# Performance work log

Measured on AMD Instinct MI355X. Metric: run time of the kernel, lower is better.

The kernel has to match this reference:

```python
import jax, jax.numpy as jnp
import numpy as np

D = 1024
H = 16
HD = D // H
FF = 4096
EPS = 1e-5
B, L = 8, 1024

def setup_inputs() -> dict:
    key = jax.random.key(0)
    ks = jax.random.split(key, 12)
    s = lambda k, shape: jax.random.normal(k, shape, dtype=jnp.float32) * (shape[0] ** -0.5)
    return {
        "x": jax.random.normal(ks[0], (B, L, D), dtype=jnp.float32),
        "attention_mask": jnp.ones((B, L), dtype=jnp.int32),
        "wq": s(ks[1], (D, D)), "bq": jnp.zeros((D,), jnp.float32),
        "wk": s(ks[2], (D, D)), "bk": jnp.zeros((D,), jnp.float32),
        "wv": s(ks[3], (D, D)), "bv": jnp.zeros((D,), jnp.float32),
        "wo": s(ks[4], (D, D)), "bo": jnp.zeros((D,), jnp.float32),
        "ln1_s": jnp.ones((D,), jnp.float32), "ln1_b": jnp.zeros((D,), jnp.float32),
        "ln2_s": jnp.ones((D,), jnp.float32), "ln2_b": jnp.zeros((D,), jnp.float32),
        "w1": s(ks[5], (D, FF)), "b1": jnp.zeros((FF,), jnp.float32),
        "w2": s(ks[6], (FF, D)), "b2": jnp.zeros((D,), jnp.float32),
    }

def _layer_norm(x, scale, bias):
    mu = jnp.mean(x, axis=-1, keepdims=True)
    var = jnp.mean(jnp.square(x - mu), axis=-1, keepdims=True)
    return (x - mu) * jax.lax.rsqrt(var + EPS) * scale + bias

def _quick_gelu(x):
    return x * jax.nn.sigmoid(1.702 * x)

def reference(x, attention_mask, wq, bq, wk, bk, wv, bv, wo, bo,
              ln1_s, ln1_b, ln2_s, ln2_b, w1, b1, w2, b2):
    Bc, Lc, Dc = x.shape
    scale = HD ** -0.5
    # --- attention block (pre-LN) ---
    h = _layer_norm(x, ln1_s, ln1_b)
    to_heads = lambda t: t.reshape(Bc, Lc, H, HD).transpose(0, 2, 1, 3)
    q = to_heads(h @ wq + bq)
    k = to_heads(h @ wk + bk)
    v = to_heads(h @ wv + bv)
    scores = jnp.einsum('bhqd,bhkd->bhqk', q.astype(jnp.float32), k.astype(jnp.float32)) * scale
    fmask = jnp.where(attention_mask[:, None, None, :] > 0, 0.0,
                      jnp.finfo(scores.dtype).min)
    weights = jax.nn.softmax(scores + fmask, axis=-1)
    attn = jnp.einsum('bhqk,bhkd->bhqd', weights, v.astype(jnp.float32))
    attn = attn.transpose(0, 2, 1, 3).reshape(Bc, Lc, Dc).astype(x.dtype)
    x = x + (attn @ wo + bo)
    # --- MLP block (pre-LN) ---
    h = _layer_norm(x, ln2_s, ln2_b)
    h = _quick_gelu(h @ w1 + b1) @ w2 + b2
    return x + h
```

## Files before the change

### kernel.cpp

```cpp
#include <hip/hip_runtime.h>
#include <math.h>

#define D_MODEL 1024
#define N_TOK   8192
#define SEQ_L   1024
#define N_HEAD  16
#define HEAD_D  64
#define FF_DIM  4096

typedef __attribute__((ext_vector_type(8))) short bf16x8;
typedef __attribute__((ext_vector_type(4))) short short4v;
typedef __attribute__((ext_vector_type(2))) int  int2v;
typedef __attribute__((ext_vector_type(4))) float f32x4;

#define MFMA16(a, b, c) __builtin_amdgcn_mfma_f32_16x16x32_bf16((a), (b), (c), 0, 0, 0)

#define GLD16(gp, lp) __builtin_amdgcn_global_load_lds(                      \
    (const __attribute__((address_space(1))) void*)(gp),                     \
    (__attribute__((address_space(3))) void*)(lp), 16, 0, 0)

#if defined(__has_builtin)
#if __has_builtin(__builtin_amdgcn_exp2f)
#define EXP2F(x) __builtin_amdgcn_exp2f(x)
#else
#define EXP2F(x) exp2f(x)
#endif
#else
#define EXP2F(x) exp2f(x)
#endif

__device__ __forceinline__ short f2bf(float f) {
    unsigned u = __float_as_uint(f);
    u += 0x7fffu + ((u >> 16) & 1u);
    return (short)(u >> 16);
}

__device__ __forceinline__ int pack2bf(float a, float b) {
    unsigned ua = __float_as_uint(a) + 0x8000u;
    unsigned ub = __float_as_uint(b) + 0x8000u;
    return __builtin_amdgcn_perm(ub, ua, 0x07060302u);
}

__global__ __launch_bounds__(256) void ln_kernel(const float* __restrict__ x,
                                                 const float* __restrict__ g,
                                                 const float* __restrict__ b,
                                                 short* __restrict__ o)
{
    int t = blockIdx.x;
    const float* xr = x + (size_t)t * D_MODEL;
    short* orow = o + (size_t)t * D_MODEL;
    float vals[4];
    float lsum = 0.f, lsq = 0.f;
#pragma unroll
    for (int i = 0; i < 4; i++) {
        float v = xr[threadIdx.x + i * 256];
        vals[i] = v; lsum += v; lsq += v * v;
    }
#pragma unroll
    for (int off = 32; off > 0; off >>= 1) {
        lsum += __shfl_down(lsum, off);
        lsq  += __shfl_down(lsq,  off);
    }
    __shared__ float red[8];
    int wid = threadIdx.x >> 6, lane = threadIdx.x & 63;
    if (lane == 0) { red[wid] = lsum; red[4 + wid] = lsq; }
    __syncthreads();
    if (threadIdx.x == 0) {
        red[0] = red[0] + red[1] + red[2] + red[3];
        red[4] = red[4] + red[5] + red[6] + red[7];
    }
    __syncthreads();
    float mean = red[0] * (1.f / D_MODEL);
    float var  = red[4] * (1.f / D_MODEL) - mean * mean;
    float inv  = rsqrtf(var + 1e-5f);
#pragma unroll
    for (int i = 0; i < 4; i++) {
        int c = threadIdx.x + i * 256;
        orow[c] = f2bf((vals[i] - mean) * inv * g[c] + b[c]);
    }
}

__global__ __launch_bounds__(256) void prep_kernel(
    const float* __restrict__ wq, const float* __restrict__ wk,
    const float* __restrict__ wv, const float* __restrict__ wo,
    const float* __restrict__ w1, const float* __restrict__ w2,
    const int*   __restrict__ amask,
    short* __restrict__ wqkvt, short* __restrict__ wot,
    short* __restrict__ w1t,  short* __restrict__ w2t,
    float* __restrict__ fmask)
{
    int id = blockIdx.x;
    if (id >= 12288) {
        int i = (id - 12288) * 256 + threadIdx.x;
        fmask[i] = (amask[i] > 0) ? 0.f : -1e30f;
        return;
    }
    const float* src; short* dst; int R, C, tloc, csh;
    if (id < 4096) {
        int wsel = id >> 10; tloc = id & 1023; R = 1024; C = 1024; csh = 5;
        src = (wsel == 0) ? wq : (wsel == 1) ? wk : (wsel == 2) ? wv : wo;
        dst = (wsel == 3) ? wot : (wqkvt + (size_t)wsel * 1024 * 1024);
    } else if (id < 8192) {
        tloc = id - 4096; R = 1024; C = 4096; csh = 7; src = w1; dst = w1t;
    } else {
        tloc = id - 8192; R = 4096; C = 1024; csh = 5; src = w2; dst = w2t;
    }
    int ty = tloc >> csh, tx = tloc & ((1 << csh) - 1);
    int r0 = ty * 32, c0 = tx * 32;
    __shared__ float t[32][33];
    int tid = threadIdx.x;
#pragma unroll
    for (int i = 0; i < 4; i++) {
        int idx = i * 256 + tid;
        int r = idx >> 5, c = idx & 31;
        t[r][c] = src[(size_t)(r0 + r) * C + c0 + c];
    }
    __syncthreads();
#pragma unroll
    for (int i = 0; i < 4; i++) {
        int idx = i * 256 + tid;
        int rr = idx >> 5, cc = idx & 31;
        dst[(size_t)(c0 + rr) * R + r0 + cc] = f2bf(t[cc][rr]);
    }
}

template<int DBUF>
__global__ __launch_bounds__(256) void gemm_bf16(
    const short* __restrict__ A, int lda,
    const short* __restrict__ Bt, int ldb,
    const float* __restrict__ bias,
    const float* __restrict__ bias2,
    const float* __restrict__ bias3,
    const float* __restrict__ resid,
    float* __restrict__ Cf, short* __restrict__ Cb, short* __restrict__ Cvt,
    int ldc, int K, int act, int qkv, int gx)
{
    __shared__ __align__(16) short sA[(1 + DBUF) * 8192];
    __shared__ __align__(16) short sB[(1 + DBUF) * 8192];
    const int tid = threadIdx.x;
    const int lane = tid & 63, wave = tid >> 6;
    const int quad = lane >> 4, l15 = lane & 15;

    const int id = blockIdx.x;
    const int xcd = id & 7, j = id >> 3;
    const int bx = j % gx, by = xcd + 8 * (j / gx);
    const int bm = by * 128, bn = bx * 128;
    const int wm = (wave >> 1) * 64, wn = (wave & 1) * 64;

    const int lr = lane >> 3;
    const int lc = (lane & 7) ^ lr;
    const int sw = l15 & 7;

    const short* Ab = A  + (size_t)(bm + wave * 32 + lr) * lda + lc * 8;
    const short* Bb = Bt + (size_t)(bn + wave * 32 + lr) * ldb + lc * 8;

    f32x4 acc[4][4];
#pragma unroll
    for (int i = 0; i < 4; i++)
#pragma unroll
        for (int jj = 0; jj < 4; jj++) acc[i][jj] = (f32x4){0.f, 0.f, 0.f, 0.f};

    const int nk = K >> 6;

    if (DBUF) {
#pragma unroll
        for (int c = 0; c < 4; c++) {
            int cid = wave * 4 + c;
            GLD16(Ab + (size_t)(c * 8) * lda, &sA[cid * 512]);
            GLD16(Bb + (size_t)(c * 8) * ldb, &sB[cid * 512]);
        }
    }

    for (int ki = 0; ki < nk; ki++) {
        __syncthreads();
        if (DBUF) {
            if (ki + 1 < nk) {
                int k0 = (ki + 1) << 6, nb = (ki + 1) & 1;
#pragma unroll
                for (int c = 0; c < 4; c++) {
                    int cid = wave * 4 + c;
                    GLD16(Ab + (size_t)(c * 8) * lda + k0, &sA[nb * 8192 + cid * 512]);
                    GLD16(Bb + (size_t)(c * 8) * ldb + k0, &sB[nb * 8192 + cid * 512]);
                }
            }
        } else {
            int k0 = ki << 6;
#pragma unroll
            for (int c = 0; c < 4; c++) {
                int cid = wave * 4 + c;
                GLD16(Ab + (size_t)(c * 8) * lda + k0, &sA[cid * 512]);
                GLD16(Bb + (size_t)(c * 8) * ldb + k0, &sB[cid * 512]);
            }
            __syncthreads();
        }
        const short* cA = &sA[DBUF ? (ki & 1) * 8192 : 0];
        const short* cB = &sB[DBUF ? (ki & 1) * 8192 : 0];
#pragma unroll
        for (int ko = 0; ko < 2; ko++) {
            bf16x8 af[4], bfr[4];
#pragma unroll
            for (int mt = 0; mt < 4; mt++) {
                int row = wm + mt * 16 + l15;
                af[mt] = *(const bf16x8*)&cA[(row * 8 + ((ko * 4 + quad) ^ sw)) * 8];
            }
#pragma unroll
            for (int nt = 0; nt < 4; nt++) {
                int row = wn + nt * 16 + l15;
                bfr[nt] = *(const bf16x8*)&cB[(row * 8 + ((ko * 4 + quad) ^ sw)) * 8];
            }
#pragma unroll
            for (int mt = 0; mt < 4; mt++)
#pragma unroll
                for (int nt = 0; nt < 4; nt++)
                    acc[mt][nt] = MFMA16(af[mt], bfr[nt], acc[mt][nt]);
        }
    }

#pragma unroll
    for (int mt = 0; mt < 4; mt++)
#pragma unroll
        for (int nt = 0; nt < 4; nt++) {
            int row0 = bm + wm + mt * 16 + quad * 4;
            int col  = bn + wn + nt * 16 + l15;
            if (qkv) {
                int seg = col >> 10, cloc = col & 1023;
                const float* bp = (seg == 0) ? bias : (seg == 1) ? bias2 : bias3;
                float bval = bp[cloc];
                if (seg == 2) {
                    int bb = row0 >> 10, l0 = row0 & 1023;
                    size_t page = (size_t)(bb * N_HEAD + (cloc >> 6)) * HEAD_D + (cloc & 63);
                    short4v pk = { f2bf(acc[mt][nt][0] + bval), f2bf(acc[mt][nt][1] + bval),
                                   f2bf(acc[mt][nt][2] + bval), f2bf(acc[mt][nt][3] + bval) };
                    *(short4v*)&Cvt[page * SEQ_L + l0] = pk;
                } else {
                    short* dst = Cb + (size_t)seg * ((size_t)N_TOK * D_MODEL);
#pragma unroll
                    for (int r = 0; r < 4; r++)
                        dst[(size_t)(row0 + r) * D_MODEL + cloc] = f2bf(acc[mt][nt][r] + bval);
                }
            } else {
#pragma unroll
                for (int r = 0; r < 4; r++) {
                    int row = row0 + r;
                    float v = acc[mt][nt][r] + bias[col];
                    if (act) v = v / (1.f + __expf(-1.702f * v));
                    if (resid) v += resid[(size_t)row * ldc + col];
                    if (Cb) Cb[(size_t)row * ldc + col] = f2bf(v);
                    else    Cf[(size_t)row * ldc + col] = v;
                }
            }
        }
}

__global__ __launch_bounds__(256) void attn_kernel(
    const short* __restrict__ Q, const short* __restrict__ Kb,
    const short* __restrict__ Vt, const float* __restrict__ fmask,
    short* __restrict__ O)
{
    __shared__ __align__(16) short sK[8192];
    __shared__ __align__(16) short sV[8192];
    __shared__ __align__(16) short sP[4][16 * 136];
    __shared__ __align__(16) float sAl[4][20];

    const int g = blockIdx.x;
    const int xcd = g & 7, slot = g >> 3;
    const int qt = slot & 15, bhl = slot >> 4;
    const int bh = xcd * 16 + bhl;
    const int b = bh >> 4, h = bh & 15;

    const int tid = threadIdx.x;
    const int wave = tid >> 6, lane = tid & 63;
    const int quad = lane >> 4, l15 = lane & 15;

    const int qbase = b * SEQ_L + qt * 64;
    const short* qp = Q + (size_t)(qbase + wave * 16 + l15) * D_MODEL + h * HEAD_D + quad * 8;
    bf16x8 qf0 = *(const bf16x8*)qp;
    bf16x8 qf1 = *(const bf16x8*)(qp + 32);

    const short* Kbh = Kb + (size_t)b * SEQ_L * D_MODEL + h * HEAD_D;
    const short* Vbh = Vt + (size_t)(b * N_HEAD + h) * HEAD_D * SEQ_L;
    const float* mk  = fmask + b * SEQ_L;

    f32x4 o4[4];
#pragma unroll
    for (int nt = 0; nt < 4; nt++) o4[nt] = (f32x4){0.f, 0.f, 0.f, 0.f};
    float mrow = -1e30f, lrow = 0.f;
    short* pslab = &sP[wave][0];
    const float CSC = 0.125f * 1.4426950408889634f;

    for (int kt = 0; kt < SEQ_L / 128; kt++) {
        __syncthreads();
#pragma unroll
        for (int j = 0; j < 4; j++) {
            int cid = wave * 4 + j;
            int kc = cid >> 1, key0 = (cid & 1) << 6;
            GLD16(Kbh + (size_t)(kt * 128 + key0 + lane) * D_MODEL + kc * 8,
                  &sK[cid * 512]);
            GLD16(Vbh + (size_t)lane * SEQ_L + kt * 128 + cid * 8,
                  &sV[cid * 512]);
        }
        __syncthreads();

        f32x4 mkv[8];
#pragma unroll
        for (int sub = 0; sub < 8; sub++)
            mkv[sub] = *(const f32x4*)&mk[kt * 128 + sub * 16 + quad * 4];

        f32x4 s[8];
#pragma unroll
        for (int sub = 0; sub < 8; sub++) {
            bf16x8 kf0 = *(const bf16x8*)&sK[(quad * 128 + sub * 16 + l15) * 8];
            bf16x8 kf1 = *(const bf16x8*)&sK[((quad + 4) * 128 + sub * 16 + l15) * 8];
            s[sub] = (f32x4){0.f, 0.f, 0.f, 0.f};
            s[sub] = MFMA16(kf0, qf0, s[sub]);
            s[sub] = MFMA16(kf1, qf1, s[sub]);
        }
#pragma unroll
        for (int sub = 0; sub < 8; sub++)
#pragma unroll
            for (int r = 0; r < 4; r++) s[sub][r] = s[sub][r] * CSC + mkv[sub][r];

        f32x4 mx4 = s[0];
#pragma unroll
        for (int sub = 1; sub < 8; sub++)
#pragma unroll
            for (int r = 0; r < 4; r++) mx4[r] = fmaxf(mx4[r], s[sub][r]);
        float pmax = fmaxf(fmaxf(mx4[0], mx4[1]), fmaxf(mx4[2], mx4[3]));
        pmax = fmaxf(pmax, __shfl_xor(pmax, 16));
        pmax = fmaxf(pmax, __shfl_xor(pmax, 32));
        float mnew = fmaxf(mrow, pmax);
        float alpha = EXP2F(mrow - mnew);
        mrow = mnew;
        if (quad == 0) sAl[wave][l15] = alpha;

        float ls = 0.f;
#pragma unroll
        for (int sub = 0; sub < 8; sub++) {
            float p0 = EXP2F(s[sub][0] - mnew);
            float p1 = EXP2F(s[sub][1] - mnew);
            float p2 = EXP2F(s[sub][2] - mnew);
            float p3 = EXP2F(s[sub][3] - mnew);
            ls += (p0 + p1) + (p2 + p3);
            int2v pk = { pack2bf(p0, p1), pack2bf(p2, p3) };
            *(int2v*)&pslab[l15 * 136 + sub * 16 + quad * 4] = pk;
        }
        ls += __shfl_xor(ls, 16);
        ls += __shfl_xor(ls, 32);
        lrow = lrow * alpha + ls;

        f32x4 av = *(const f32x4*)&sAl[wave][quad * 4];
#pragma unroll
        for (int nt = 0; nt < 4; nt++)
#pragma unroll
            for (int r = 0; r < 4; r++) o4[nt][r] *= av[r];

        bf16x8 pf[4];
#pragma unroll
        for (int c = 0; c < 4; c++)
            pf[c] = *(const bf16x8*)&pslab[l15 * 136 + c * 32 + quad * 8];
#pragma unroll
        for (int nt = 0; nt < 4; nt++)
#pragma unroll
            for (int c = 0; c < 4; c++) {
                bf16x8 vfr = *(const bf16x8*)&sV[((c * 4 + quad) * 64 + nt * 16 + l15) * 8];
                o4[nt] = MFMA16(pf[c], vfr, o4[nt]);
            }
    }
    if (quad == 0) sAl[wave][l15] = 1.f / lrow;
    __syncthreads();
    f32x4 iv = *(const f32x4*)&sAl[wave][quad * 4];
#pragma unroll
    for (int nt = 0; nt < 4; nt++)
#pragma unroll
        for (int r = 0; r < 4; r++)
            O[(size_t)(qbase + wave * 16 + quad * 4 + r) * D_MODEL
              + h * HEAD_D + nt * 16 + l15] = f2bf(o4[nt][r] * iv[r]);
}

extern "C" void kernel_launch(void* const* d_in, const int* in_sizes, int n_in,
                              void* d_out, int out_size, void* d_ws, size_t ws_size,
                              hipStream_t stream)
{
    const float* x     = (const float*)d_in[0];
    const int*   amask = (const int*)  d_in[1];
    const float* wq    = (const float*)d_in[2];
    const float* bq    = (const float*)d_in[3];
    const float* wk    = (const float*)d_in[4];
    const float* bk    = (const float*)d_in[5];
    const float* wv    = (const float*)d_in[6];
    const float* bv    = (const float*)d_in[7];
    const float* wo    = (const float*)d_in[8];
    const float* bo    = (const float*)d_in[9];
    const float* ln1s  = (const float*)d_in[10];
    const float* ln1b  = (const float*)d_in[11];
    const float* ln2s  = (const float*)d_in[12];
    const float* ln2b  = (const float*)d_in[13];
    const float* w1    = (const float*)d_in[14];
    const float* b1    = (const float*)d_in[15];
    const float* w2    = (const float*)d_in[16];
    const float* b2    = (const float*)d_in[17];
    float* out = (float*)d_out;

    char* w = (char*)d_ws;
    short* wqkvt = (short*)(w + (size_t)0);
    short* wot   = (short*)(w + ((size_t)6  << 20));
    short* w1t   = (short*)(w + ((size_t)8  << 20));
    short* w2t   = (short*)(w + ((size_t)16 << 20));
    short* hb    = (short*)(w + ((size_t)24 << 20));
    short* qb    = (short*)(w + ((size_t)40 << 20));
    short* kbf   = (short*)(w + ((size_t)56 << 20));
    short* attnb = (short*)(w + ((size_t)72 << 20));
    short* vtb   = (short*)(w + ((size_t)88 << 20));
    short* ffb   = qb;
    float* fmaskb = (float*)d_out;

    dim3 blk(256);

    prep_kernel<<<dim3(12320), blk, 0, stream>>>(wq, wk, wv, wo, w1, w2, amask,
                                                 wqkvt, wot, w1t, w2t, fmaskb);

    ln_kernel<<<N_TOK, blk, 0, stream>>>(x, ln1s, ln1b, hb);

    gemm_bf16<0><<<dim3(24 * 64), blk, 0, stream>>>(
        hb, 1024, wqkvt, 1024, bq, bk, bv, nullptr,
        nullptr, qb, vtb, 1024, 1024, 0, 1, 24);

    attn_kernel<<<dim3(2048), blk, 0, stream>>>(qb, kbf, vtb, fmaskb, attnb);

    gemm_bf16<1><<<dim3(8 * 64), blk, 0, stream>>>(
        attnb, 1024, wot, 1024, bo, nullptr, nullptr, x,
        out, nullptr, nullptr, 1024, 1024, 0, 0, 8);

    ln_kernel<<<N_TOK, blk, 0, stream>>>(out, ln2s, ln2b, hb);

    gemm_bf16<0><<<dim3(32 * 64), blk, 0, stream>>>(
        hb, 1024, w1t, 1024, b1, nullptr, nullptr, nullptr,
        nullptr, ffb, nullptr, 4096, 1024, 1, 0, 32);
    gemm_bf16<1><<<dim3(8 * 64), blk, 0, stream>>>(
        ffb, 4096, w2t, 4096, b2, nullptr, nullptr, out,
        out, nullptr, nullptr, 1024, 4096, 0, 0, 8);
}
```

Measured before the change: 554.8 us.

## Process two 16-row query tiles per wave in attention kernel

Each wave now handles 32 query rows instead of 16, so the block covers 128 queries and the grid halves to 1024 blocks. Every K/V tile loaded into shared memory and every K/V fragment read from LDS is reused for two query tiles, which halves the global K/V traffic and LDS fragment reads per query. The cost is more accumulator and score registers per thread (possibly lower occupancy), a larger P slab in shared memory, and fewer blocks to fill the GPU.

```diff
diff --git a/kernel.cpp b/kernel.cpp
--- a/kernel.cpp
+++ b/kernel.cpp
@@ -259,12 +259,12 @@
 {
     __shared__ __align__(16) short sK[8192];
     __shared__ __align__(16) short sV[8192];
-    __shared__ __align__(16) short sP[4][16 * 136];
-    __shared__ __align__(16) float sAl[4][20];
+    __shared__ __align__(16) short sP[4][32 * 136];
+    __shared__ __align__(16) float sAl[4][2][20];
 
     const int g = blockIdx.x;
     const int xcd = g & 7, slot = g >> 3;
-    const int qt = slot & 15, bhl = slot >> 4;
+    const int qt = slot & 7, bhl = slot >> 3;
     const int bh = xcd * 16 + bhl;
     const int b = bh >> 4, h = bh & 15;
 
@@ -272,19 +272,26 @@
     const int wave = tid >> 6, lane = tid & 63;
     const int quad = lane >> 4, l15 = lane & 15;
 
-    const int qbase = b * SEQ_L + qt * 64;
-    const short* qp = Q + (size_t)(qbase + wave * 16 + l15) * D_MODEL + h * HEAD_D + quad * 8;
-    bf16x8 qf0 = *(const bf16x8*)qp;
-    bf16x8 qf1 = *(const bf16x8*)(qp + 32);
+    const int qbase = b * SEQ_L + qt * 128;
+    bf16x8 qf[2][2];
+#pragma unroll
+    for (int qh = 0; qh < 2; qh++) {
+        const short* qp = Q + (size_t)(qbase + wave * 32 + qh * 16 + l15) * D_MODEL
+                        + h * HEAD_D + quad * 8;
+        qf[qh][0] = *(const bf16x8*)qp;
+        qf[qh][1] = *(const bf16x8*)(qp + 32);
+    }
 
     const short* Kbh = Kb + (size_t)b * SEQ_L * D_MODEL + h * HEAD_D;
     const short* Vbh = Vt + (size_t)(b * N_HEAD + h) * HEAD_D * SEQ_L;
     const float* mk  = fmask + b * SEQ_L;
 
-    f32x4 o4[4];
-#pragma unroll
-    for (int nt = 0; nt < 4; nt++) o4[nt] = (f32x4){0.f, 0.f, 0.f, 0.f};
-    float mrow = -1e30f, lrow = 0.f;
+    f32x4 o4[2][4];
+#pragma unroll
+    for (int qh = 0; qh < 2; qh++)
+#pragma unroll
+        for (int nt = 0; nt < 4; nt++) o4[qh][nt] = (f32x4){0.f, 0.f, 0.f, 0.f};
+    float mrow[2] = {-1e30f, -1e30f}, lrow[2] = {0.f, 0.f};
     short* pslab = &sP[wave][0];
     const float CSC = 0.125f * 1.4426950408889634f;
 
@@ -306,75 +313,94 @@
         for (int sub = 0; sub < 8; sub++)
             mkv[sub] = *(const f32x4*)&mk[kt * 128 + sub * 16 + quad * 4];
 
-        f32x4 s[8];
+        f32x4 s[8][2];
 #pragma unroll
         for (int sub = 0; sub < 8; sub++) {
             bf16x8 kf0 = *(const bf16x8*)&sK[(quad * 128 + sub * 16 + l15) * 8];
             bf16x8 kf1 = *(const bf16x8*)&sK[((quad + 4) * 128 + sub * 16 + l15) * 8];
-            s[sub] = (f32x4){0.f, 0.f, 0.f, 0.f};
-            s[sub] = MFMA16(kf0, qf0, s[sub]);
-            s[sub] = MFMA16(kf1, qf1, s[sub]);
-        }
-#pragma unroll
-        for (int sub = 0; sub < 8; sub++)
-#pragma unroll
-            for (int r = 0; r < 4; r++) s[sub][r] = s[sub][r] * CSC + mkv[sub][r];
-
-        f32x4 mx4 = s[0];
-#pragma unroll
-        for (int sub = 1; sub < 8; sub++)
-#pragma unroll
-            for (int r = 0; r < 4; r++) mx4[r] = fmaxf(mx4[r], s[sub][r]);
-        float pmax = fmaxf(fmaxf(mx4[0], mx4[1]), fmaxf(mx4[2], mx4[3]));
-        pmax = fmaxf(pmax, __shfl_xor(pmax, 16));
-        pmax = fmaxf(pmax, __shfl_xor(pmax, 32));
-        float mnew = fmaxf(mrow, pmax);
-        float alpha = EXP2F(mrow - mnew);
-        mrow = mnew;
-        if (quad == 0) sAl[wave][l15] = alpha;
-
-        float ls = 0.f;
-#pragma unroll
-        for (int sub = 0; sub < 8; sub++) {
-            float p0 = EXP2F(s[sub][0] - mnew);
-            float p1 = EXP2F(s[sub][1] - mnew);
-            float p2 = EXP2F(s[sub][2] - mnew);
-            float p3 = EXP2F(s[sub][3] - mnew);
-            ls += (p0 + p1) + (p2 + p3);
-            int2v pk = { pack2bf(p0, p1), pack2bf(p2, p3) };
-            *(int2v*)&pslab[l15 * 136 + sub * 16 + quad * 4] = pk;
-        }
-        ls += __shfl_xor(ls, 16);
-        ls += __shfl_xor(ls, 32);
-        lrow = lrow * alpha + ls;
-
-        f32x4 av = *(const f32x4*)&sAl[wave][quad * 4];
-#pragma unroll
-        for (int nt = 0; nt < 4; nt++)
-#pragma unroll
-            for (int r = 0; r < 4; r++) o4[nt][r] *= av[r];
-
-        bf16x8 pf[4];
-#pragma unroll
-        for (int c = 0; c < 4; c++)
-            pf[c] = *(const bf16x8*)&pslab[l15 * 136 + c * 32 + quad * 8];
+#pragma unroll
+            for (int qh = 0; qh < 2; qh++) {
+                s[sub][qh] = (f32x4){0.f, 0.f, 0.f, 0.f};
+                s[sub][qh] = MFMA16(kf0, qf[qh][0], s[sub][qh]);
+                s[sub][qh] = MFMA16(kf1, qf[qh][1], s[sub][qh]);
+            }
+        }
+        float alpha[2];
+#pragma unroll
+        for (int qh = 0; qh < 2; qh++) {
+#pragma unroll
+            for (int sub = 0; sub < 8; sub++)
+#pragma unroll
+                for (int r = 0; r < 4; r++)
+                    s[sub][qh][r] = s[sub][qh][r] * CSC + mkv[sub][r];
+            f32x4 mx4 = s[0][qh];
+#pragma unroll
+            for (int sub = 1; sub < 8; sub++)
+#pragma unroll
+                for (int r = 0; r < 4; r++) mx4[r] = fmaxf(mx4[r], s[sub][qh][r]);
+            float pmax = fmaxf(fmaxf(mx4[0], mx4[1]), fmaxf(mx4[2], mx4[3]));
+            pmax = fmaxf(pmax, __shfl_xor(pmax, 16));
+            pmax = fmaxf(pmax, __shfl_xor(pmax, 32));
+            float mnew = fmaxf(mrow[qh], pmax);
+            alpha[qh] = EXP2F(mrow[qh] - mnew);
+            mrow[qh] = mnew;
+            if (quad == 0) sAl[wave][qh][l15] = alpha[qh];
+
+            float ls = 0.f;
+#pragma unroll
+            for (int sub = 0; sub < 8; sub++) {
+                float p0 = EXP2F(s[sub][qh][0] - mnew);
+                float p1 = EXP2F(s[sub][qh][1] - mnew);
+                float p2 = EXP2F(s[sub][qh][2] - mnew);
+                float p3 = EXP2F(s[sub][qh][3] - mnew);
+                ls += (p0 + p1) + (p2 + p3);
+                int2v pk = { pack2bf(p0, p1), pack2bf(p2, p3) };
+                *(int2v*)&pslab[(qh * 16 + l15) * 136 + sub * 16 + quad * 4] = pk;
+            }
+            ls += __shfl_xor(ls, 16);
+            ls += __shfl_xor(ls, 32);
+            lrow[qh] = lrow[qh] * alpha[qh] + ls;
+        }
+
+#pragma unroll
+        for (int qh = 0; qh < 2; qh++) {
+            f32x4 av = *(const f32x4*)&sAl[wave][qh][quad * 4];
+#pragma unroll
+            for (int nt = 0; nt < 4; nt++)
+#pragma unroll
+                for (int r = 0; r < 4; r++) o4[qh][nt][r] *= av[r];
+        }
+
+        bf16x8 pf[2][4];
+#pragma unroll
+        for (int qh = 0; qh < 2; qh++)
+#pragma unroll
+            for (int c = 0; c < 4; c++)
+                pf[qh][c] = *(const bf16x8*)&pslab[(qh * 16 + l15) * 136 + c * 32 + quad * 8];
 #pragma unroll
         for (int nt = 0; nt < 4; nt++)
 #pragma unroll
             for (int c = 0; c < 4; c++) {
                 bf16x8 vfr = *(const bf16x8*)&sV[((c * 4 + quad) * 64 + nt * 16 + l15) * 8];
-                o4[nt] = MFMA16(pf[c], vfr, o4[nt]);
-            }
-    }
-    if (quad == 0) sAl[wave][l15] = 1.f / lrow;
+                o4[0][nt] = MFMA16(pf[0][c], vfr, o4[0][nt]);
+                o4[1][nt] = MFMA16(pf[1][c], vfr, o4[1][nt]);
+            }
+    }
+    if (quad == 0) {
+        sAl[wave][0][l15] = 1.f / lrow[0];
+        sAl[wave][1][l15] = 1.f / lrow[1];
+    }
     __syncthreads();
-    f32x4 iv = *(const f32x4*)&sAl[wave][quad * 4];
-#pragma unroll
-    for (int nt = 0; nt < 4; nt++)
-#pragma unroll
-        for (int r = 0; r < 4; r++)
-            O[(size_t)(qbase + wave * 16 + quad * 4 + r) * D_MODEL
-              + h * HEAD_D + nt * 16 + l15] = f2bf(o4[nt][r] * iv[r]);
+#pragma unroll
+    for (int qh = 0; qh < 2; qh++) {
+        f32x4 iv = *(const f32x4*)&sAl[wave][qh][quad * 4];
+#pragma unroll
+        for (int nt = 0; nt < 4; nt++)
+#pragma unroll
+            for (int r = 0; r < 4; r++)
+                O[(size_t)(qbase + wave * 32 + qh * 16 + quad * 4 + r) * D_MODEL
+                  + h * HEAD_D + nt * 16 + l15] = f2bf(o4[qh][nt][r] * iv[r]);
+    }
 }
 
 extern "C" void kernel_launch(void* const* d_in, const int* in_sizes, int n_in,
@@ -425,7 +451,7 @@
         hb, 1024, wqkvt, 1024, bq, bk, bv, nullptr,
         nullptr, qb, vtb, 1024, 1024, 0, 1, 24);
 
-    attn_kernel<<<dim3(2048), blk, 0, stream>>>(qb, kbf, vtb, fmaskb, attnb);
+    attn_kernel<<<dim3(1024), blk, 0, stream>>>(qb, kbf, vtb, fmaskb, attnb);
 
     gemm_bf16<1><<<dim3(8 * 64), blk, 0, stream>>>(
         attnb, 1024, wot, 1024, bo, nullptr, nullptr, x,
```

Result: faster. 536.7 us (-3.3%).
